# Kernel optimization log

Measured on AMD Instinct MI355X. Metric: run time of the kernel, lower is better.

Reference implementation:

```python
import jax, jax.numpy as jnp
from jax import lax
import numpy as np

B, T, E, H = 64, 512, 1024, 1024

def setup_inputs() -> dict:
    key = jax.random.key(0)
    k1, k2, k3, k4, k5, k6 = jax.random.split(key, 6)
    s = 1.0 / np.sqrt(H)  # torch LSTM init scale
    embeddings = jax.random.normal(k1, (B, T, E), dtype=jnp.float32)
    seq_lengths = jax.random.randint(k2, (B,), 1, T + 1)
    W_ih = jax.random.uniform(k3, (4 * H, E), minval=-s, maxval=s, dtype=jnp.float32)
    W_hh = jax.random.uniform(k4, (4 * H, H), minval=-s, maxval=s, dtype=jnp.float32)
    b_ih = jax.random.uniform(k5, (4 * H,), minval=-s, maxval=s, dtype=jnp.float32)
    b_hh = jax.random.uniform(k6, (4 * H,), minval=-s, maxval=s, dtype=jnp.float32)
    return {"embeddings": embeddings, "seq_lengths": seq_lengths,
            "W_ih": W_ih, "W_hh": W_hh, "b_ih": b_ih, "b_hh": b_hh}

def _lstm_outputs(embeddings, W_ih, W_hh, b_ih, b_hh):
    x = jnp.swapaxes(embeddings, 0, 1)  # [T, B, E] (time-major, as nn.LSTM batch_first=False)
    # Hoist the input projection into one big GEMM: [T,B,4H]
    x_proj = jnp.einsum('tbe,ge->tbg', x, W_ih) + b_ih + b_hh

    def step(carry, xp):
        h, c = carry
        gates = xp + h @ W_hh.T                      # [B, 4H]
        i, f, g, o = jnp.split(gates, 4, axis=-1)    # torch gate order: i, f, g, o
        i = jax.nn.sigmoid(i)
        f = jax.nn.sigmoid(f)
        g = jnp.tanh(g)
        o = jax.nn.sigmoid(o)
        c = f * c + i * g
        h = o * jnp.tanh(c)
        return (h, c), h

    h0 = jnp.zeros((x.shape[1], W_hh.shape[1]), x.dtype)
    _, outs = lax.scan(step, (h0, h0), x_proj)       # outs: [T, B, H]
    return outs

def reference(embeddings, seq_lengths, W_ih, W_hh, b_ih, b_hh):
    outs = _lstm_outputs(embeddings, W_ih, W_hh, b_ih, b_hh)  # [T, B, H]
    t = outs.shape[0]
    idx = (seq_lengths - 1) % t                      # wraps like python negative indexing
    repr_ = outs[idx, jnp.arange(outs.shape[1])]     # [B, H]
    return repr_
```

## Files before the change

### kernel.cpp

```cpp
#include <hip/hip_runtime.h>
#include <stdint.h>


typedef _Float16 half8 __attribute__((ext_vector_type(8)));
typedef _Float16 half4_ __attribute__((ext_vector_type(4)));
typedef float f32x4 __attribute__((ext_vector_type(4)));
typedef unsigned int u32x4 __attribute__((ext_vector_type(4)));

#define T_SEQ 512

__global__ void k_f32_to_f16(const float* __restrict__ s, _Float16* __restrict__ d, int n4) {
  int i = blockIdx.x * blockDim.x + threadIdx.x;
  if (i >= n4) return;
  f32x4 v = ((const f32x4*)s)[i];
  half4_ h;
  h.x = (_Float16)v.x; h.y = (_Float16)v.y; h.z = (_Float16)v.z; h.w = (_Float16)v.w;
  ((half4_*)d)[i] = h;
}

__global__ void k_bias_sum(const float* __restrict__ a, const float* __restrict__ b,
                           float* __restrict__ o) {
  int i = blockIdx.x * blockDim.x + threadIdx.x;
  if (i < 4096) o[i] = a[i] + b[i];
}

__global__ __launch_bounds__(256, 2) void k_gemm_xproj(
    const _Float16* __restrict__ X, const _Float16* __restrict__ W,
    const float* __restrict__ bsum, _Float16* __restrict__ C) {
  __shared__ _Float16 As[128 * 64];
  __shared__ _Float16 Bs[128 * 64];
  const int bid = blockIdx.x;
  const int ntile = bid & 31, mtile = bid >> 5;
  const int tid = threadIdx.x;
  const int wave = tid >> 6, lane = tid & 63;
  const int wr = wave >> 1, wc = wave & 1;
  const int R0 = lane >> 3, cg = lane & 7;

  f32x4 acc[4][4];
#pragma unroll
  for (int m = 0; m < 4; m++)
#pragma unroll
    for (int n = 0; n < 4; n++) acc[m][n] = (f32x4){0.f, 0.f, 0.f, 0.f};

  for (int k0 = 0; k0 < 1024; k0 += 64) {
#pragma unroll
    for (int i = 0; i < 4; i++) {
      const int rr = (wave * 4 + i) * 8 + R0;
      const _Float16* ga = X + (size_t)(mtile * 128 + rr) * 1024 + k0 + ((cg ^ (rr & 7)) * 8);
      const _Float16* gb = W + (size_t)(ntile * 128 + rr) * 1024 + k0 + ((cg ^ (rr & 7)) * 8);
      __builtin_amdgcn_global_load_lds(
          (const __attribute__((address_space(1))) void*)ga,
          (__attribute__((address_space(3))) void*)((char*)As + (wave * 4 + i) * 1024), 16, 0, 0);
      __builtin_amdgcn_global_load_lds(
          (const __attribute__((address_space(1))) void*)gb,
          (__attribute__((address_space(3))) void*)((char*)Bs + (wave * 4 + i) * 1024), 16, 0, 0);
    }
    asm volatile("s_waitcnt vmcnt(0)" ::: "memory");
    __syncthreads();
#pragma unroll
    for (int kk = 0; kk < 2; kk++) {
      half8 af[4], bf[4];
#pragma unroll
      for (int m = 0; m < 4; m++) {
        int r = wr * 64 + m * 16 + (lane & 15);
        af[m] = *(const half8*)((const char*)As + r * 128 +
                                (((kk * 4 + (lane >> 4)) ^ (r & 7)) << 4));
      }
#pragma unroll
      for (int n = 0; n < 4; n++) {
        int r = wc * 64 + n * 16 + (lane & 15);
        bf[n] = *(const half8*)((const char*)Bs + r * 128 +
                                (((kk * 4 + (lane >> 4)) ^ (r & 7)) << 4));
      }
#pragma unroll
      for (int m = 0; m < 4; m++)
#pragma unroll
        for (int n = 0; n < 4; n++)
          acc[m][n] = __builtin_amdgcn_mfma_f32_16x16x32_f16(af[m], bf[n], acc[m][n], 0, 0, 0);
    }
    __syncthreads();
  }
#pragma unroll
  for (int n = 0; n < 4; n++) {
    int col = ntile * 128 + wc * 64 + n * 16 + (lane & 15);
    float bs = bsum[col];
#pragma unroll
    for (int m = 0; m < 4; m++)
#pragma unroll
      for (int q = 0; q < 4; q++) {
        int row = mtile * 128 + wr * 64 + m * 16 + (lane >> 4) * 4 + q;
        int bb = row >> 9, tt = row & 511;
        C[((size_t)tt * 64 + bb) * 4096 + col] = (_Float16)(acc[m][n][q] + bs);
      }
  }
}

__global__ __launch_bounds__(256, 1) void k_lstm_rec(
    const _Float16* __restrict__ Whh,
    const _Float16* __restrict__ xprojT,
    const int* __restrict__ seqlen,
    unsigned* __restrict__ hbuf,
    float* __restrict__ out) {
  __shared__ _Float16 h_lds[16 * 1024];
  __shared__ float gates[64 * 17];

  const int bid = blockIdx.x;
  const int x8 = bid & 7;
  const int g = x8 >> 1;
  const int s = (x8 & 1) * 32 + (bid >> 3);
  const int tid = threadIdx.x;
  const int wave = tid >> 6, lane = tid & 63;

  for (int i = tid; i < 4096; i += 256) ((uint64_t*)h_lds)[i] = 0ull;

  half8 wfrag[32];
  {
    const _Float16* wp =
        Whh + (size_t)(1024 * wave + s * 16 + (lane & 15)) * 1024 + (lane >> 4) * 8;
#pragma unroll
    for (int kk = 0; kk < 32; kk++) wfrag[kk] = *(const half8*)(wp + kk * 32);
  }

  int Lg = 1;
  for (int b = 0; b < 16; b++) {
    int L = seqlen[g * 16 + b];
    Lg = L > Lg ? L : Lg;
  }
  const int be = tid >> 4, ue = tid & 15;
  const int mylen = seqlen[g * 16 + be];
  float c_state = 0.f;

  const int rowbase = (lane & 15) * 2048;
  const int xorm = ((lane & 15) & 7) << 4;

  __syncthreads();

  for (int t = 0; t < Lg; t++) {
    float xp[4];
#pragma unroll
    for (int q = 0; q < 4; q++) {
      int bm = (lane >> 4) * 4 + q;
      xp[q] = (float)xprojT[((size_t)t * 64 + g * 16 + bm) * 4096 + 1024 * wave + s * 16 +
                            (lane & 15)];
    }

    if (t > 0) {
      const unsigned* src = hbuf + ((size_t)(t & 1)) * 65536 + (size_t)g * 16384;
      const unsigned Etag = (unsigned)t << 16;
#pragma unroll
      for (int hf = 0; hf < 2; hf++) {
        u32x4 hv[8];
        unsigned done = 0;
        while (done != 0xFFu) {
#pragma unroll
          for (int i = 0; i < 8; i++) {
            if (!(done & (1u << i))) {
              asm volatile("global_load_dwordx4 %0, %1, off sc0 sc1"
                           : "=v"(hv[i])
                           : "v"(src + (size_t)(tid + ((hf * 8 + i) << 8)) * 4)
                           : "memory");
            }
          }
          asm volatile("s_waitcnt vmcnt(0)" ::: "memory");
#pragma unroll
          for (int i = 0; i < 8; i++) {
            if (!(done & (1u << i))) {
              unsigned m = ((hv[i].x ^ Etag) | (hv[i].y ^ Etag) | (hv[i].z ^ Etag) |
                            (hv[i].w ^ Etag)) & 0xFFFF0000u;
              if (__all(m == 0u)) done |= 1u << i;
            }
          }
        }
#pragma unroll
        for (int i = 0; i < 8; i++) {
          int ch = tid + ((hf * 8 + i) << 8);
          int br = ch >> 8, cidx = ch & 255;
          unsigned lo = (hv[i].x & 0xFFFFu) | (hv[i].y << 16);
          unsigned hi = (hv[i].z & 0xFFFFu) | (hv[i].w << 16);
          *(uint64_t*)((char*)h_lds + br * 2048 + (((cidx >> 1) ^ (br & 7)) << 4) +
                       (cidx & 1) * 8) = (uint64_t)lo | ((uint64_t)hi << 32);
        }
      }
    }
    __syncthreads();

    f32x4 a0 = (f32x4){0.f, 0.f, 0.f, 0.f};
    f32x4 a1 = (f32x4){0.f, 0.f, 0.f, 0.f};
    f32x4 a2 = (f32x4){0.f, 0.f, 0.f, 0.f};
    f32x4 a3 = (f32x4){0.f, 0.f, 0.f, 0.f};
    const char* lb = (const char*)h_lds + rowbase;
#pragma unroll
    for (int kk = 0; kk < 32; kk += 4) {
      half8 f0 = *(const half8*)(lb + ((((kk + 0) * 4 + (lane >> 4)) << 4) ^ xorm));
      half8 f1 = *(const half8*)(lb + ((((kk + 1) * 4 + (lane >> 4)) << 4) ^ xorm));
      half8 f2 = *(const half8*)(lb + ((((kk + 2) * 4 + (lane >> 4)) << 4) ^ xorm));
      half8 f3 = *(const half8*)(lb + ((((kk + 3) * 4 + (lane >> 4)) << 4) ^ xorm));
      a0 = __builtin_amdgcn_mfma_f32_16x16x32_f16(f0, wfrag[kk + 0], a0, 0, 0, 0);
      a1 = __builtin_amdgcn_mfma_f32_16x16x32_f16(f1, wfrag[kk + 1], a1, 0, 0, 0);
      a2 = __builtin_amdgcn_mfma_f32_16x16x32_f16(f2, wfrag[kk + 2], a2, 0, 0, 0);
      a3 = __builtin_amdgcn_mfma_f32_16x16x32_f16(f3, wfrag[kk + 3], a3, 0, 0, 0);
    }
    {
      f32x4 gv4;
#pragma unroll
      for (int q = 0; q < 4; q++) gv4[q] = (a0[q] + a1[q]) + (a2[q] + a3[q]) + xp[q];
      *(f32x4*)&gates[(wave * 16 + (lane & 15)) * 17 + (lane >> 4) * 4] = gv4;
    }
    __syncthreads();

    float iv = gates[(0 + ue) * 17 + be];
    float fv = gates[(16 + ue) * 17 + be];
    float gv = gates[(32 + ue) * 17 + be];
    float ov = gates[(48 + ue) * 17 + be];
    iv = 1.f / (1.f + __expf(-iv));
    fv = 1.f / (1.f + __expf(-fv));
    gv = 1.f - 2.f / (1.f + __expf(2.f * gv));
    ov = 1.f / (1.f + __expf(-ov));
    c_state = fv * c_state + iv * gv;
    float tc = 1.f - 2.f / (1.f + __expf(2.f * c_state));
    float hv = ov * tc;
    if (t + 1 == mylen) out[(size_t)(g * 16 + be) * 1024 + s * 16 + ue] = hv;

    if (t + 1 < Lg) {
      _Float16 hfv = (_Float16)hv;
      unsigned short hb;
      __builtin_memcpy(&hb, &hfv, 2);
      unsigned tw = ((unsigned)(t + 1) << 16) | (unsigned)hb;
      __hip_atomic_store(hbuf + ((size_t)((t + 1) & 1)) * 65536 +
                             (size_t)(g * 16 + be) * 1024 + s * 16 + ue,
                         tw, __ATOMIC_RELAXED, __HIP_MEMORY_SCOPE_AGENT);
    }
  }
}

extern "C" void kernel_launch(void* const* d_in, const int* in_sizes, int n_in, void* d_out,
                              int out_size, void* d_ws, size_t ws_size, hipStream_t stream) {
  const float* emb = (const float*)d_in[0];
  const int* slen = (const int*)d_in[1];
  const float* Wih = (const float*)d_in[2];
  const float* Whh = (const float*)d_in[3];
  const float* bih = (const float*)d_in[4];
  const float* bhh = (const float*)d_in[5];
  float* out = (float*)d_out;

  char* ws = (char*)d_ws;
  _Float16* xprojT = (_Float16*)(ws + 0);
  _Float16* xf = (_Float16*)(ws + 268435456);
  unsigned* hbuf = (unsigned*)(ws + 268435456);
  _Float16* wihf = (_Float16*)(ws + 335544320);
  _Float16* whhf = (_Float16*)(ws + 343932928);
  float* bsum = (float*)(ws + 352321536);

  k_f32_to_f16<<<(8388608 + 255) / 256, 256, 0, stream>>>(emb, xf, 8388608);
  k_f32_to_f16<<<(1048576 + 255) / 256, 256, 0, stream>>>(Wih, wihf, 1048576);
  k_f32_to_f16<<<(1048576 + 255) / 256, 256, 0, stream>>>(Whh, whhf, 1048576);
  k_bias_sum<<<16, 256, 0, stream>>>(bih, bhh, bsum);
  k_gemm_xproj<<<8192, 256, 0, stream>>>(xf, wihf, bsum, xprojT);
  hipMemsetAsync(hbuf, 0, 524288, stream);
  k_lstm_rec<<<256, 256, 0, stream>>>(whhf, xprojT, slen, hbuf, out);
}
```

Measured before the change: 1.947 ms.

## Halve recurrent blocks to 512 threads and overlap h-polling with first-half MFMAs

The persistent LSTM recurrence now runs 128 blocks of 512 threads, each owning 32 hidden units instead of 16. That halves the number of blocks taking part in the cross-block flag-polling exchange each step. Each step's h fetch is split in two halves: the first half of the K-dimension MFMAs starts once the first half of h is in LDS, while the second half is still being verified and stored. This aims to hide part of the global-memory handshake latency behind compute, at the cost of an extra __syncthreads per step and larger blocks, which need enough registers for two per CU.

```diff
diff --git a/kernel.cpp b/kernel.cpp
--- a/kernel.cpp
+++ b/kernel.cpp
@@ -6,8 +6,6 @@
 typedef _Float16 half4_ __attribute__((ext_vector_type(4)));
 typedef float f32x4 __attribute__((ext_vector_type(4)));
 typedef unsigned int u32x4 __attribute__((ext_vector_type(4)));
-
-#define T_SEQ 512
 
 __global__ void k_f32_to_f16(const float* __restrict__ s, _Float16* __restrict__ d, int n4) {
   int i = blockIdx.x * blockDim.x + threadIdx.x;
@@ -95,28 +93,28 @@
   }
 }
 
-__global__ __launch_bounds__(256, 1) void k_lstm_rec(
+__global__ __launch_bounds__(512, 2) void k_lstm_rec(
     const _Float16* __restrict__ Whh,
     const _Float16* __restrict__ xprojT,
     const int* __restrict__ seqlen,
     unsigned* __restrict__ hbuf,
     float* __restrict__ out) {
   __shared__ _Float16 h_lds[16 * 1024];
-  __shared__ float gates[64 * 17];
+  __shared__ float gates[128 * 17];
 
   const int bid = blockIdx.x;
-  const int x8 = bid & 7;
-  const int g = x8 >> 1;
-  const int s = (x8 & 1) * 32 + (bid >> 3);
+  const int g = (bid & 7) >> 1;
+  const int s32 = (bid & 1) * 16 + (bid >> 3);
   const int tid = threadIdx.x;
   const int wave = tid >> 6, lane = tid & 63;
-
-  for (int i = tid; i < 4096; i += 256) ((uint64_t*)h_lds)[i] = 0ull;
+  const int G = wave >> 1, uh = wave & 1;
+
+  for (int i = tid; i < 4096; i += 512) ((uint64_t*)h_lds)[i] = 0ull;
 
   half8 wfrag[32];
   {
-    const _Float16* wp =
-        Whh + (size_t)(1024 * wave + s * 16 + (lane & 15)) * 1024 + (lane >> 4) * 8;
+    const _Float16* wp = Whh +
+        (size_t)(1024 * G + s32 * 32 + uh * 16 + (lane & 15)) * 1024 + (lane >> 4) * 8;
 #pragma unroll
     for (int kk = 0; kk < 32; kk++) wfrag[kk] = *(const half8*)(wp + kk * 32);
   }
@@ -126,12 +124,14 @@
     int L = seqlen[g * 16 + b];
     Lg = L > Lg ? L : Lg;
   }
-  const int be = tid >> 4, ue = tid & 15;
+  const int be = tid >> 5, ue = tid & 31;
   const int mylen = seqlen[g * 16 + be];
   float c_state = 0.f;
 
   const int rowbase = (lane & 15) * 2048;
   const int xorm = ((lane & 15) & 7) << 4;
+  const int br = tid & 15;
+  const int uc0 = tid >> 4;
 
   __syncthreads();
 
@@ -140,45 +140,50 @@
 #pragma unroll
     for (int q = 0; q < 4; q++) {
       int bm = (lane >> 4) * 4 + q;
-      xp[q] = (float)xprojT[((size_t)t * 64 + g * 16 + bm) * 4096 + 1024 * wave + s * 16 +
-                            (lane & 15)];
-    }
-
+      xp[q] = (float)xprojT[((size_t)t * 64 + g * 16 + bm) * 4096 + 1024 * G + s32 * 32 +
+                            uh * 16 + (lane & 15)];
+    }
+
+    u32x4 hv[8];
     if (t > 0) {
       const unsigned* src = hbuf + ((size_t)(t & 1)) * 65536 + (size_t)g * 16384;
       const unsigned Etag = (unsigned)t << 16;
 #pragma unroll
-      for (int hf = 0; hf < 2; hf++) {
-        u32x4 hv[8];
+      for (int i = 0; i < 8; i++) {
+        asm volatile("global_load_dwordx4 %0, %1, off sc0 sc1"
+                     : "=v"(hv[i]) : "v"(src + (size_t)br * 1024 + (uc0 + (i << 5)) * 4)
+                     : "memory");
+      }
+      asm volatile("s_waitcnt vmcnt(0)" ::: "memory");
+      {
         unsigned done = 0;
-        while (done != 0xFFu) {
-#pragma unroll
-          for (int i = 0; i < 8; i++) {
-            if (!(done & (1u << i))) {
-              asm volatile("global_load_dwordx4 %0, %1, off sc0 sc1"
-                           : "=v"(hv[i])
-                           : "v"(src + (size_t)(tid + ((hf * 8 + i) << 8)) * 4)
-                           : "memory");
-            }
-          }
-          asm volatile("s_waitcnt vmcnt(0)" ::: "memory");
-#pragma unroll
-          for (int i = 0; i < 8; i++) {
+        for (;;) {
+#pragma unroll
+          for (int i = 0; i < 4; i++) {
             if (!(done & (1u << i))) {
               unsigned m = ((hv[i].x ^ Etag) | (hv[i].y ^ Etag) | (hv[i].z ^ Etag) |
                             (hv[i].w ^ Etag)) & 0xFFFF0000u;
               if (__all(m == 0u)) done |= 1u << i;
             }
           }
+          if (done == 0xFu) break;
+#pragma unroll
+          for (int i = 0; i < 4; i++) {
+            if (!(done & (1u << i))) {
+              asm volatile("global_load_dwordx4 %0, %1, off sc0 sc1"
+                           : "=v"(hv[i]) : "v"(src + (size_t)br * 1024 + (uc0 + (i << 5)) * 4)
+                           : "memory");
+            }
+          }
+          asm volatile("s_waitcnt vmcnt(0)" ::: "memory");
         }
 #pragma unroll
-        for (int i = 0; i < 8; i++) {
-          int ch = tid + ((hf * 8 + i) << 8);
-          int br = ch >> 8, cidx = ch & 255;
+        for (int i = 0; i < 4; i++) {
+          int uc = uc0 + (i << 5);
           unsigned lo = (hv[i].x & 0xFFFFu) | (hv[i].y << 16);
           unsigned hi = (hv[i].z & 0xFFFFu) | (hv[i].w << 16);
-          *(uint64_t*)((char*)h_lds + br * 2048 + (((cidx >> 1) ^ (br & 7)) << 4) +
-                       (cidx & 1) * 8) = (uint64_t)lo | ((uint64_t)hi << 32);
+          *(uint64_t*)((char*)h_lds + br * 2048 + (((uc >> 1) ^ (br & 7)) << 4) +
+                       (uc & 1) * 8) = (uint64_t)lo | ((uint64_t)hi << 32);
         }
       }
     }
@@ -186,48 +191,87 @@
 
     f32x4 a0 = (f32x4){0.f, 0.f, 0.f, 0.f};
     f32x4 a1 = (f32x4){0.f, 0.f, 0.f, 0.f};
+    const char* lb = (const char*)h_lds + rowbase;
+#pragma unroll
+    for (int kk = 0; kk < 16; kk += 2) {
+      half8 f0 = *(const half8*)(lb + ((((kk + 0) * 4 + (lane >> 4)) << 4) ^ xorm));
+      half8 f1 = *(const half8*)(lb + ((((kk + 1) * 4 + (lane >> 4)) << 4) ^ xorm));
+      a0 = __builtin_amdgcn_mfma_f32_16x16x32_f16(f0, wfrag[kk + 0], a0, 0, 0, 0);
+      a1 = __builtin_amdgcn_mfma_f32_16x16x32_f16(f1, wfrag[kk + 1], a1, 0, 0, 0);
+    }
+
+    if (t > 0) {
+      const unsigned* src = hbuf + ((size_t)(t & 1)) * 65536 + (size_t)g * 16384;
+      const unsigned Etag = (unsigned)t << 16;
+      unsigned done = 0;
+      for (;;) {
+#pragma unroll
+        for (int i = 4; i < 8; i++) {
+          if (!(done & (1u << i))) {
+            unsigned m = ((hv[i].x ^ Etag) | (hv[i].y ^ Etag) | (hv[i].z ^ Etag) |
+                          (hv[i].w ^ Etag)) & 0xFFFF0000u;
+            if (__all(m == 0u)) done |= 1u << i;
+          }
+        }
+        if (done == 0xF0u) break;
+#pragma unroll
+        for (int i = 4; i < 8; i++) {
+          if (!(done & (1u << i))) {
+            asm volatile("global_load_dwordx4 %0, %1, off sc0 sc1"
+                         : "=v"(hv[i]) : "v"(src + (size_t)br * 1024 + (uc0 + (i << 5)) * 4)
+                         : "memory");
+          }
+        }
+        asm volatile("s_waitcnt vmcnt(0)" ::: "memory");
+      }
+#pragma unroll
+      for (int i = 4; i < 8; i++) {
+        int uc = uc0 + (i << 5);
+        unsigned lo = (hv[i].x & 0xFFFFu) | (hv[i].y << 16);
+        unsigned hi = (hv[i].z & 0xFFFFu) | (hv[i].w << 16);
+        *(uint64_t*)((char*)h_lds + br * 2048 + (((uc >> 1) ^ (br & 7)) << 4) +
+                     (uc & 1) * 8) = (uint64_t)lo | ((uint64_t)hi << 32);
+      }
+    }
+    __syncthreads();
+
     f32x4 a2 = (f32x4){0.f, 0.f, 0.f, 0.f};
     f32x4 a3 = (f32x4){0.f, 0.f, 0.f, 0.f};
-    const char* lb = (const char*)h_lds + rowbase;
-#pragma unroll
-    for (int kk = 0; kk < 32; kk += 4) {
+#pragma unroll
+    for (int kk = 16; kk < 32; kk += 2) {
       half8 f0 = *(const half8*)(lb + ((((kk + 0) * 4 + (lane >> 4)) << 4) ^ xorm));
       half8 f1 = *(const half8*)(lb + ((((kk + 1) * 4 + (lane >> 4)) << 4) ^ xorm));
-      half8 f2 = *(const half8*)(lb + ((((kk + 2) * 4 + (lane >> 4)) << 4) ^ xorm));
-      half8 f3 = *(const half8*)(lb + ((((kk + 3) * 4 + (lane >> 4)) << 4) ^ xorm));
-      a0 = __builtin_amdgcn_mfma_f32_16x16x32_f16(f0, wfrag[kk + 0], a0, 0, 0, 0);
-      a1 = __builtin_amdgcn_mfma_f32_16x16x32_f16(f1, wfrag[kk + 1], a1, 0, 0, 0);
-      a2 = __builtin_amdgcn_mfma_f32_16x16x32_f16(f2, wfrag[kk + 2], a2, 0, 0, 0);
-      a3 = __builtin_amdgcn_mfma_f32_16x16x32_f16(f3, wfrag[kk + 3], a3, 0, 0, 0);
+      a2 = __builtin_amdgcn_mfma_f32_16x16x32_f16(f0, wfrag[kk + 0], a2, 0, 0, 0);
+      a3 = __builtin_amdgcn_mfma_f32_16x16x32_f16(f1, wfrag[kk + 1], a3, 0, 0, 0);
     }
     {
       f32x4 gv4;
 #pragma unroll
       for (int q = 0; q < 4; q++) gv4[q] = (a0[q] + a1[q]) + (a2[q] + a3[q]) + xp[q];
-      *(f32x4*)&gates[(wave * 16 + (lane & 15)) * 17 + (lane >> 4) * 4] = gv4;
+      *(f32x4*)&gates[(G * 32 + uh * 16 + (lane & 15)) * 17 + (lane >> 4) * 4] = gv4;
     }
     __syncthreads();
 
     float iv = gates[(0 + ue) * 17 + be];
-    float fv = gates[(16 + ue) * 17 + be];
-    float gv = gates[(32 + ue) * 17 + be];
-    float ov = gates[(48 + ue) * 17 + be];
+    float fv = gates[(32 + ue) * 17 + be];
+    float gv = gates[(64 + ue) * 17 + be];
+    float ov = gates[(96 + ue) * 17 + be];
     iv = 1.f / (1.f + __expf(-iv));
     fv = 1.f / (1.f + __expf(-fv));
     gv = 1.f - 2.f / (1.f + __expf(2.f * gv));
     ov = 1.f / (1.f + __expf(-ov));
     c_state = fv * c_state + iv * gv;
     float tc = 1.f - 2.f / (1.f + __expf(2.f * c_state));
-    float hv = ov * tc;
-    if (t + 1 == mylen) out[(size_t)(g * 16 + be) * 1024 + s * 16 + ue] = hv;
+    float hvv = ov * tc;
+    if (t + 1 == mylen) out[(size_t)(g * 16 + be) * 1024 + s32 * 32 + ue] = hvv;
 
     if (t + 1 < Lg) {
-      _Float16 hfv = (_Float16)hv;
+      _Float16 hf16 = (_Float16)hvv;
       unsigned short hb;
-      __builtin_memcpy(&hb, &hfv, 2);
+      __builtin_memcpy(&hb, &hf16, 2);
       unsigned tw = ((unsigned)(t + 1) << 16) | (unsigned)hb;
       __hip_atomic_store(hbuf + ((size_t)((t + 1) & 1)) * 65536 +
-                             (size_t)(g * 16 + be) * 1024 + s * 16 + ue,
+                             (size_t)(g * 16 + be) * 1024 + s32 * 32 + ue,
                          tw, __ATOMIC_RELAXED, __HIP_MEMORY_SCOPE_AGENT);
     }
   }
@@ -257,5 +301,5 @@
   k_bias_sum<<<16, 256, 0, stream>>>(bih, bhh, bsum);
   k_gemm_xproj<<<8192, 256, 0, stream>>>(xf, wihf, bsum, xprojT);
   hipMemsetAsync(hbuf, 0, 524288, stream);
-  k_lstm_rec<<<256, 256, 0, stream>>>(whhf, xprojT, slen, hbuf, out);
-}
+  k_lstm_rec<<<128, 512, 0, stream>>>(whhf, xprojT, slen, hbuf, out);
+}
```

Result: slower. 3.409 ms (+75.1%).

## Halve recurrent LSTM blocks by giving each 512-thread block 32 hidden units

Applied to the files above, without the earlier changes.

The recurrent kernel now uses 128 blocks of 512 threads instead of 256 blocks of 256, so each block computes 32 hidden units per batch group (eight waves, two per gate). The number of blocks exchanging h through global memory each step drops by half, and each block's polling read of the shared h slice is issued as one batch of 8 loads before the retry loop. This cuts the global-memory polling traffic and synchronization fan-in per timestep. In exchange, each step runs 8-wave block barriers and keeps the weight fragments in registers for 512 threads, which may raise register pressure under the new launch bounds.

```diff
diff --git a/kernel.cpp b/kernel.cpp
--- a/kernel.cpp
+++ b/kernel.cpp
@@ -6,8 +6,6 @@
 typedef _Float16 half4_ __attribute__((ext_vector_type(4)));
 typedef float f32x4 __attribute__((ext_vector_type(4)));
 typedef unsigned int u32x4 __attribute__((ext_vector_type(4)));
-
-#define T_SEQ 512
 
 __global__ void k_f32_to_f16(const float* __restrict__ s, _Float16* __restrict__ d, int n4) {
   int i = blockIdx.x * blockDim.x + threadIdx.x;
@@ -95,28 +93,28 @@
   }
 }
 
-__global__ __launch_bounds__(256, 1) void k_lstm_rec(
+__global__ __launch_bounds__(512, 2) void k_lstm_rec(
     const _Float16* __restrict__ Whh,
     const _Float16* __restrict__ xprojT,
     const int* __restrict__ seqlen,
     unsigned* __restrict__ hbuf,
     float* __restrict__ out) {
   __shared__ _Float16 h_lds[16 * 1024];
-  __shared__ float gates[64 * 17];
+  __shared__ float gates[128 * 17];
 
   const int bid = blockIdx.x;
-  const int x8 = bid & 7;
-  const int g = x8 >> 1;
-  const int s = (x8 & 1) * 32 + (bid >> 3);
+  const int g = (bid & 7) >> 1;
+  const int s32 = (bid & 1) * 16 + (bid >> 3);
   const int tid = threadIdx.x;
   const int wave = tid >> 6, lane = tid & 63;
-
-  for (int i = tid; i < 4096; i += 256) ((uint64_t*)h_lds)[i] = 0ull;
+  const int G = wave >> 1, uh = wave & 1;
+
+  for (int i = tid; i < 4096; i += 512) ((uint64_t*)h_lds)[i] = 0ull;
 
   half8 wfrag[32];
   {
-    const _Float16* wp =
-        Whh + (size_t)(1024 * wave + s * 16 + (lane & 15)) * 1024 + (lane >> 4) * 8;
+    const _Float16* wp = Whh +
+        (size_t)(1024 * G + s32 * 32 + uh * 16 + (lane & 15)) * 1024 + (lane >> 4) * 8;
 #pragma unroll
     for (int kk = 0; kk < 32; kk++) wfrag[kk] = *(const half8*)(wp + kk * 32);
   }
@@ -126,7 +124,7 @@
     int L = seqlen[g * 16 + b];
     Lg = L > Lg ? L : Lg;
   }
-  const int be = tid >> 4, ue = tid & 15;
+  const int be = tid >> 5, ue = tid & 31;
   const int mylen = seqlen[g * 16 + be];
   float c_state = 0.f;
 
@@ -140,46 +138,48 @@
 #pragma unroll
     for (int q = 0; q < 4; q++) {
       int bm = (lane >> 4) * 4 + q;
-      xp[q] = (float)xprojT[((size_t)t * 64 + g * 16 + bm) * 4096 + 1024 * wave + s * 16 +
-                            (lane & 15)];
+      xp[q] = (float)xprojT[((size_t)t * 64 + g * 16 + bm) * 4096 + 1024 * G + s32 * 32 +
+                            uh * 16 + (lane & 15)];
     }
 
     if (t > 0) {
       const unsigned* src = hbuf + ((size_t)(t & 1)) * 65536 + (size_t)g * 16384;
       const unsigned Etag = (unsigned)t << 16;
-#pragma unroll
-      for (int hf = 0; hf < 2; hf++) {
-        u32x4 hv[8];
-        unsigned done = 0;
-        while (done != 0xFFu) {
-#pragma unroll
-          for (int i = 0; i < 8; i++) {
-            if (!(done & (1u << i))) {
-              asm volatile("global_load_dwordx4 %0, %1, off sc0 sc1"
-                           : "=v"(hv[i])
-                           : "v"(src + (size_t)(tid + ((hf * 8 + i) << 8)) * 4)
-                           : "memory");
-            }
-          }
-          asm volatile("s_waitcnt vmcnt(0)" ::: "memory");
-#pragma unroll
-          for (int i = 0; i < 8; i++) {
-            if (!(done & (1u << i))) {
-              unsigned m = ((hv[i].x ^ Etag) | (hv[i].y ^ Etag) | (hv[i].z ^ Etag) |
-                            (hv[i].w ^ Etag)) & 0xFFFF0000u;
-              if (__all(m == 0u)) done |= 1u << i;
-            }
+      u32x4 hv[8];
+#pragma unroll
+      for (int i = 0; i < 8; i++) {
+        asm volatile("global_load_dwordx4 %0, %1, off sc0 sc1"
+                     : "=v"(hv[i]) : "v"(src + (size_t)(tid + (i << 9)) * 4) : "memory");
+      }
+      asm volatile("s_waitcnt vmcnt(0)" ::: "memory");
+      unsigned done = 0;
+      for (;;) {
+#pragma unroll
+        for (int i = 0; i < 8; i++) {
+          if (!(done & (1u << i))) {
+            unsigned m = ((hv[i].x ^ Etag) | (hv[i].y ^ Etag) | (hv[i].z ^ Etag) |
+                          (hv[i].w ^ Etag)) & 0xFFFF0000u;
+            if (__all(m == 0u)) done |= 1u << i;
           }
         }
+        if (done == 0xFFu) break;
 #pragma unroll
         for (int i = 0; i < 8; i++) {
-          int ch = tid + ((hf * 8 + i) << 8);
-          int br = ch >> 8, cidx = ch & 255;
-          unsigned lo = (hv[i].x & 0xFFFFu) | (hv[i].y << 16);
-          unsigned hi = (hv[i].z & 0xFFFFu) | (hv[i].w << 16);
-          *(uint64_t*)((char*)h_lds + br * 2048 + (((cidx >> 1) ^ (br & 7)) << 4) +
-                       (cidx & 1) * 8) = (uint64_t)lo | ((uint64_t)hi << 32);
+          if (!(done & (1u << i))) {
+            asm volatile("global_load_dwordx4 %0, %1, off sc0 sc1"
+                         : "=v"(hv[i]) : "v"(src + (size_t)(tid + (i << 9)) * 4) : "memory");
+          }
         }
+        asm volatile("s_waitcnt vmcnt(0)" ::: "memory");
+      }
+#pragma unroll
+      for (int i = 0; i < 8; i++) {
+        int ch = tid + (i << 9);
+        int br = ch >> 8, cidx = ch & 255;
+        unsigned lo = (hv[i].x & 0xFFFFu) | (hv[i].y << 16);
+        unsigned hi = (hv[i].z & 0xFFFFu) | (hv[i].w << 16);
+        *(uint64_t*)((char*)h_lds + br * 2048 + (((cidx >> 1) ^ (br & 7)) << 4) +
+                     (cidx & 1) * 8) = (uint64_t)lo | ((uint64_t)hi << 32);
       }
     }
     __syncthreads();
@@ -204,30 +204,30 @@
       f32x4 gv4;
 #pragma unroll
       for (int q = 0; q < 4; q++) gv4[q] = (a0[q] + a1[q]) + (a2[q] + a3[q]) + xp[q];
-      *(f32x4*)&gates[(wave * 16 + (lane & 15)) * 17 + (lane >> 4) * 4] = gv4;
+      *(f32x4*)&gates[(G * 32 + uh * 16 + (lane & 15)) * 17 + (lane >> 4) * 4] = gv4;
     }
     __syncthreads();
 
     float iv = gates[(0 + ue) * 17 + be];
-    float fv = gates[(16 + ue) * 17 + be];
-    float gv = gates[(32 + ue) * 17 + be];
-    float ov = gates[(48 + ue) * 17 + be];
+    float fv = gates[(32 + ue) * 17 + be];
+    float gv = gates[(64 + ue) * 17 + be];
+    float ov = gates[(96 + ue) * 17 + be];
     iv = 1.f / (1.f + __expf(-iv));
     fv = 1.f / (1.f + __expf(-fv));
     gv = 1.f - 2.f / (1.f + __expf(2.f * gv));
     ov = 1.f / (1.f + __expf(-ov));
     c_state = fv * c_state + iv * gv;
     float tc = 1.f - 2.f / (1.f + __expf(2.f * c_state));
-    float hv = ov * tc;
-    if (t + 1 == mylen) out[(size_t)(g * 16 + be) * 1024 + s * 16 + ue] = hv;
+    float hvv = ov * tc;
+    if (t + 1 == mylen) out[(size_t)(g * 16 + be) * 1024 + s32 * 32 + ue] = hvv;
 
     if (t + 1 < Lg) {
-      _Float16 hfv = (_Float16)hv;
+      _Float16 hf16 = (_Float16)hvv;
       unsigned short hb;
-      __builtin_memcpy(&hb, &hfv, 2);
+      __builtin_memcpy(&hb, &hf16, 2);
       unsigned tw = ((unsigned)(t + 1) << 16) | (unsigned)hb;
       __hip_atomic_store(hbuf + ((size_t)((t + 1) & 1)) * 65536 +
-                             (size_t)(g * 16 + be) * 1024 + s * 16 + ue,
+                             (size_t)(g * 16 + be) * 1024 + s32 * 32 + ue,
                          tw, __ATOMIC_RELAXED, __HIP_MEMORY_SCOPE_AGENT);
     }
   }
@@ -257,5 +257,5 @@
   k_bias_sum<<<16, 256, 0, stream>>>(bih, bhh, bsum);
   k_gemm_xproj<<<8192, 256, 0, stream>>>(xf, wihf, bsum, xprojT);
   hipMemsetAsync(hbuf, 0, 524288, stream);
-  k_lstm_rec<<<256, 256, 0, stream>>>(whhf, xprojT, slen, hbuf, out);
-}
+  k_lstm_rec<<<128, 512, 0, stream>>>(whhf, xprojT, slen, hbuf, out);
+}
```

Result: slower. 3.094 ms (+58.9%).

## Pack hidden-state flag into fp16 LSB to halve cross-block exchange traffic

Applied to the files above, without the earlier changes.

The per-step hidden-state exchange buffer changes from 32-bit words (16-bit value plus 16-bit step tag) to 16-bit words. The low mantissa bit of each fp16 value now carries a parity flag that alternates every two steps. Each poll therefore reads half as many bytes, and the values go straight into LDS without repacking. The cost is one bit of fp16 precision in h. The flag is also weaker: it only tells steps apart modulo four within each double buffer, and the memsets seed the initial parity to match.

```diff
diff --git a/kernel.cpp b/kernel.cpp
--- a/kernel.cpp
+++ b/kernel.cpp
@@ -6,8 +6,6 @@
 typedef _Float16 half4_ __attribute__((ext_vector_type(4)));
 typedef float f32x4 __attribute__((ext_vector_type(4)));
 typedef unsigned int u32x4 __attribute__((ext_vector_type(4)));
-
-#define T_SEQ 512
 
 __global__ void k_f32_to_f16(const float* __restrict__ s, _Float16* __restrict__ d, int n4) {
   int i = blockIdx.x * blockDim.x + threadIdx.x;
@@ -99,7 +97,7 @@
     const _Float16* __restrict__ Whh,
     const _Float16* __restrict__ xprojT,
     const int* __restrict__ seqlen,
-    unsigned* __restrict__ hbuf,
+    unsigned short* __restrict__ hbuf,
     float* __restrict__ out) {
   __shared__ _Float16 h_lds[16 * 1024];
   __shared__ float gates[64 * 17];
@@ -145,41 +143,41 @@
     }
 
     if (t > 0) {
-      const unsigned* src = hbuf + ((size_t)(t & 1)) * 65536 + (size_t)g * 16384;
-      const unsigned Etag = (unsigned)t << 16;
-#pragma unroll
-      for (int hf = 0; hf < 2; hf++) {
-        u32x4 hv[8];
-        unsigned done = 0;
-        while (done != 0xFFu) {
-#pragma unroll
-          for (int i = 0; i < 8; i++) {
-            if (!(done & (1u << i))) {
-              asm volatile("global_load_dwordx4 %0, %1, off sc0 sc1"
-                           : "=v"(hv[i])
-                           : "v"(src + (size_t)(tid + ((hf * 8 + i) << 8)) * 4)
-                           : "memory");
-            }
-          }
-          asm volatile("s_waitcnt vmcnt(0)" ::: "memory");
-#pragma unroll
-          for (int i = 0; i < 8; i++) {
-            if (!(done & (1u << i))) {
-              unsigned m = ((hv[i].x ^ Etag) | (hv[i].y ^ Etag) | (hv[i].z ^ Etag) |
-                            (hv[i].w ^ Etag)) & 0xFFFF0000u;
-              if (__all(m == 0u)) done |= 1u << i;
-            }
+      const unsigned short* src = hbuf + ((size_t)(t & 1)) * 65536 + (size_t)g * 16384;
+      const unsigned pb = (((unsigned)t >> 1) & 1u) ^ 1u;
+      const unsigned exp2 = pb ? 0x00010001u : 0u;
+      u32x4 hv[8];
+#pragma unroll
+      for (int i = 0; i < 8; i++) {
+        asm volatile("global_load_dwordx4 %0, %1, off sc0 sc1"
+                     : "=v"(hv[i]) : "v"(src + (size_t)(tid + (i << 8)) * 8) : "memory");
+      }
+      asm volatile("s_waitcnt vmcnt(0)" ::: "memory");
+      unsigned done = 0;
+      for (;;) {
+#pragma unroll
+        for (int i = 0; i < 8; i++) {
+          if (!(done & (1u << i))) {
+            unsigned m = ((hv[i].x ^ exp2) | (hv[i].y ^ exp2) | (hv[i].z ^ exp2) |
+                          (hv[i].w ^ exp2)) & 0x00010001u;
+            if (__all(m == 0u)) done |= 1u << i;
           }
         }
+        if (done == 0xFFu) break;
 #pragma unroll
         for (int i = 0; i < 8; i++) {
-          int ch = tid + ((hf * 8 + i) << 8);
-          int br = ch >> 8, cidx = ch & 255;
-          unsigned lo = (hv[i].x & 0xFFFFu) | (hv[i].y << 16);
-          unsigned hi = (hv[i].z & 0xFFFFu) | (hv[i].w << 16);
-          *(uint64_t*)((char*)h_lds + br * 2048 + (((cidx >> 1) ^ (br & 7)) << 4) +
-                       (cidx & 1) * 8) = (uint64_t)lo | ((uint64_t)hi << 32);
+          if (!(done & (1u << i))) {
+            asm volatile("global_load_dwordx4 %0, %1, off sc0 sc1"
+                         : "=v"(hv[i]) : "v"(src + (size_t)(tid + (i << 8)) * 8) : "memory");
+          }
         }
+        asm volatile("s_waitcnt vmcnt(0)" ::: "memory");
+      }
+#pragma unroll
+      for (int i = 0; i < 8; i++) {
+        int ch = tid + (i << 8);
+        int br = ch >> 7, cidx = ch & 127;
+        *(u32x4*)((char*)h_lds + br * 2048 + ((cidx ^ (br & 7)) << 4)) = hv[i];
       }
     }
     __syncthreads();
@@ -222,13 +220,14 @@
     if (t + 1 == mylen) out[(size_t)(g * 16 + be) * 1024 + s * 16 + ue] = hv;
 
     if (t + 1 < Lg) {
-      _Float16 hfv = (_Float16)hv;
+      _Float16 hf = (_Float16)hv;
       unsigned short hb;
-      __builtin_memcpy(&hb, &hfv, 2);
-      unsigned tw = ((unsigned)(t + 1) << 16) | (unsigned)hb;
+      __builtin_memcpy(&hb, &hf, 2);
+      unsigned ps = (((unsigned)(t + 1) >> 1) & 1u) ^ 1u;
+      hb = (unsigned short)((hb & 0xFFFEu) | ps);
       __hip_atomic_store(hbuf + ((size_t)((t + 1) & 1)) * 65536 +
                              (size_t)(g * 16 + be) * 1024 + s * 16 + ue,
-                         tw, __ATOMIC_RELAXED, __HIP_MEMORY_SCOPE_AGENT);
+                         hb, __ATOMIC_RELAXED, __HIP_MEMORY_SCOPE_AGENT);
     }
   }
 }
@@ -246,7 +245,8 @@
   char* ws = (char*)d_ws;
   _Float16* xprojT = (_Float16*)(ws + 0);
   _Float16* xf = (_Float16*)(ws + 268435456);
-  unsigned* hbuf = (unsigned*)(ws + 268435456);
+  unsigned short* hbuf =
+      (unsigned short*)(ws + 268435456);
   _Float16* wihf = (_Float16*)(ws + 335544320);
   _Float16* whhf = (_Float16*)(ws + 343932928);
   float* bsum = (float*)(ws + 352321536);
@@ -256,6 +256,7 @@
   k_f32_to_f16<<<(1048576 + 255) / 256, 256, 0, stream>>>(Whh, whhf, 1048576);
   k_bias_sum<<<16, 256, 0, stream>>>(bih, bhh, bsum);
   k_gemm_xproj<<<8192, 256, 0, stream>>>(xf, wihf, bsum, xprojT);
-  hipMemsetAsync(hbuf, 0, 524288, stream);
+  hipMemsetAsync((char*)hbuf, 0x01, 131072, stream);
+  hipMemsetAsync((char*)hbuf + 131072, 0x00, 131072, stream);
   k_lstm_rec<<<256, 256, 0, stream>>>(whhf, xprojT, slen, hbuf, out);
 }
```

Measured after the change: 2.161 ms. 1.11x slower.
